# Kernel tuning notes

Hardware: AMD Instinct MI355X
Metric: run time of the kernel (lower is better)

## Reference

```python
import jax, jax.numpy as jnp
import numpy as np

INPUT_DIM = 768
HIDDEN = 64
NUM_CLASSES = 1


def _uniform(key, shape, bound):
    return jax.random.uniform(key, shape, jnp.float32, -bound, bound)


def setup_inputs() -> dict:
    key = jax.random.key(0)
    ks = jax.random.split(key, 16)
    B, T = 128, 512
    bound = 1.0 / np.sqrt(HIDDEN)  # PyTorch RNN init range
    inp = {
        "x": jax.random.normal(ks[0], (B, T, INPUT_DIM), jnp.float32),
        "fixation_num": 1,
        # layer 0: input_dim -> hidden
        "W_ih0": _uniform(ks[1], (HIDDEN, INPUT_DIM), bound),
        "W_hh0": _uniform(ks[2], (HIDDEN, HIDDEN), bound),
        "b_ih0": _uniform(ks[3], (HIDDEN,), bound),
        "b_hh0": _uniform(ks[4], (HIDDEN,), bound),
        # layer 1
        "W_ih1": _uniform(ks[5], (HIDDEN, HIDDEN), bound),
        "W_hh1": _uniform(ks[6], (HIDDEN, HIDDEN), bound),
        "b_ih1": _uniform(ks[7], (HIDDEN,), bound),
        "b_hh1": _uniform(ks[8], (HIDDEN,), bound),
        # layer 2
        "W_ih2": _uniform(ks[9], (HIDDEN, HIDDEN), bound),
        "W_hh2": _uniform(ks[10], (HIDDEN, HIDDEN), bound),
        "b_ih2": _uniform(ks[11], (HIDDEN,), bound),
        "b_hh2": _uniform(ks[12], (HIDDEN,), bound),
        # final linear head
        "fc_w": _uniform(ks[13], (NUM_CLASSES, HIDDEN), bound),
        "fc_b": _uniform(ks[14], (NUM_CLASSES,), bound),
    }
    return inp


def _rnn_layer(x, W_ih, W_hh, b_ih, b_hh):
    # x: [B, T, In] -> hidden sequence [B, T, H]; vanilla tanh RNN, h0 = 0
    pre = jnp.einsum("bti,hi->bth", x, W_ih) + b_ih + b_hh  # input projection for all t
    B = x.shape[0]
    h0 = jnp.zeros((B, W_hh.shape[0]), x.dtype)

    def step(h, p_t):  # p_t: [B, H]
        h = jnp.tanh(p_t + h @ W_hh.T)
        return h, h

    _, hs = jax.lax.scan(step, h0, jnp.swapaxes(pre, 0, 1))  # hs: [T, B, H]
    return jnp.swapaxes(hs, 0, 1)


def reference(x, fixation_num, W_ih0, W_hh0, b_ih0, b_hh0,
              W_ih1, W_hh1, b_ih1, b_hh1,
              W_ih2, W_hh2, b_ih2, b_hh2, fc_w, fc_b):
    # fixation_num is unused by the original forward
    h = _rnn_layer(x, W_ih0, W_hh0, b_ih0, b_hh0)
    h = _rnn_layer(h, W_ih1, W_hh1, b_ih1, b_hh1)
    h = _rnn_layer(h, W_ih2, W_hh2, b_ih2, b_hh2)
    last = h[:, -1, :]  # [B, H]
    return last @ fc_w.T + fc_b  # [B, num_classes]
```

## Files before the change

kernel.cpp:

```cpp
#include <hip/hip_runtime.h>


typedef __fp16 h2_t __attribute__((ext_vector_type(2)));
typedef __fp16 h8_t __attribute__((ext_vector_type(8)));
typedef float  f4_t __attribute__((ext_vector_type(4)));

union F4H  { float4 f; h2_t h[4]; };
union F4H8 { float4 f; h8_t h8; h2_t h2[4]; };
union H8U  { h2_t h2[4]; h8_t h8; };

__device__ __forceinline__ float fdot2(h2_t a, h2_t b, float c) {
    return __builtin_amdgcn_fdot2(a, b, c, false);
}
__device__ __forceinline__ h2_t pack_h2(float x, float y) {
    return __builtin_amdgcn_cvt_pkrtz(x, y);
}
__device__ __forceinline__ float tanh_fast(float x) {
    float e = __expf(2.0f * x);
    return 1.0f - 2.0f * __builtin_amdgcn_rcpf(e + 1.0f);
}

__global__ __launch_bounds__(256) void pack_wih(
    const float* __restrict__ W, h8_t* __restrict__ wp)
{
    const int id = blockIdx.x * 256 + threadIdx.x;
    if (id >= 24 * 4 * 64) return;
    const int l  = id & 63;
    const int nt = (id >> 6) & 3;
    const int c  = id >> 8;
    const float* p = W + (size_t)(nt * 16 + (l & 15)) * 768 + c * 32 + (l >> 4) * 8;
    float4 r0 = *(const float4*)p;
    float4 r1 = *(const float4*)(p + 4);
    H8U u;
    u.h2[0] = pack_h2(r0.x, r0.y); u.h2[1] = pack_h2(r0.z, r0.w);
    u.h2[2] = pack_h2(r1.x, r1.y); u.h2[3] = pack_h2(r1.z, r1.w);
    wp[id] = u.h8;
}

__global__ __launch_bounds__(256) void gemm_pre0(
    const float* __restrict__ x,
    const h8_t* __restrict__ wp,
    const float* __restrict__ bih, const float* __restrict__ bhh,
    float* __restrict__ pre0)
{
    const int tid = threadIdx.x;
    const int wv  = tid >> 6;
    const int l   = tid & 63;
    const int m   = l & 15;
    const int q   = l >> 4;
    const int rowB = blockIdx.x * 64 + wv * 16;

    const float* ax = x + (size_t)(rowB + m) * 768 + q * 8;

    float4 ar[2][2];
    h8_t   bf[2][4];

#pragma unroll
    for (int c = 0; c < 2; ++c) {
        ar[c][0] = *(const float4*)(ax + c * 32);
        ar[c][1] = *(const float4*)(ax + c * 32 + 4);
        const int cb = c * 256 + l;
        bf[c][0] = wp[cb];        bf[c][1] = wp[cb + 64];
        bf[c][2] = wp[cb + 128];  bf[c][3] = wp[cb + 192];
    }

    f4_t acc[4];
#pragma unroll
    for (int nt = 0; nt < 4; ++nt)
#pragma unroll
        for (int i = 0; i < 4; ++i) acc[nt][i] = 0.0f;

#pragma unroll
    for (int it = 0; it < 24; ++it) {
        const int bs = it & 1;
        H8U fa;
        fa.h2[0] = pack_h2(ar[bs][0].x, ar[bs][0].y);
        fa.h2[1] = pack_h2(ar[bs][0].z, ar[bs][0].w);
        fa.h2[2] = pack_h2(ar[bs][1].x, ar[bs][1].y);
        fa.h2[3] = pack_h2(ar[bs][1].z, ar[bs][1].w);
        h8_t fb0 = bf[bs][0], fb1 = bf[bs][1], fb2 = bf[bs][2], fb3 = bf[bs][3];

        if (it + 2 < 24) {
            const int ko = (it + 2) * 32;
            ar[bs][0] = *(const float4*)(ax + ko);
            ar[bs][1] = *(const float4*)(ax + ko + 4);
            const int cb = (it + 2) * 256 + l;
            bf[bs][0] = wp[cb];        bf[bs][1] = wp[cb + 64];
            bf[bs][2] = wp[cb + 128];  bf[bs][3] = wp[cb + 192];
        }

        acc[0] = __builtin_amdgcn_mfma_f32_16x16x32_f16(fa.h8, fb0, acc[0], 0, 0, 0);
        acc[1] = __builtin_amdgcn_mfma_f32_16x16x32_f16(fa.h8, fb1, acc[1], 0, 0, 0);
        acc[2] = __builtin_amdgcn_mfma_f32_16x16x32_f16(fa.h8, fb2, acc[2], 0, 0, 0);
        acc[3] = __builtin_amdgcn_mfma_f32_16x16x32_f16(fa.h8, fb3, acc[3], 0, 0, 0);
    }

    float bn[4];
#pragma unroll
    for (int nt = 0; nt < 4; ++nt) bn[nt] = bih[nt * 16 + m] + bhh[nt * 16 + m];
#pragma unroll
    for (int i = 0; i < 4; ++i) {
        int row = rowB + q * 4 + i;
        float* pr = pre0 + (size_t)row * 64 + m;
#pragma unroll
        for (int nt = 0; nt < 4; ++nt)
            pr[nt * 16] = acc[nt][i] + bn[nt];
    }
}

__device__ __forceinline__ float layer_epoch(
    const __fp16* __restrict__ in0,
    __fp16* __restrict__ self0, int par,
    const h2_t* wB2, const h8_t* wX, float* __restrict__ xb,
    const float* bias4, int j)
{
    __fp16*       selfPar  = self0 + par * 1024;
    const __fp16* selfPrev = self0 + (par ^ 1) * 1024;
    const int mm = j & 15;
    const int q4 = j >> 4;

    F4H8 A0, A1;
    const __fp16* arow = in0 + mm * 64 + q4 * 8;
    A0.f = *(const float4*)arow;
    A1.f = *(const float4*)(arow + 32);

    f4_t xacc[4];
#pragma unroll
    for (int nt = 0; nt < 4; ++nt) {
#pragma unroll
        for (int i = 0; i < 4; ++i) xacc[nt][i] = 0.0f;
        xacc[nt] = __builtin_amdgcn_mfma_f32_16x16x32_f16(
            A0.h8, wX[nt * 2 + 0], xacc[nt], 0, 0, 0);
        xacc[nt] = __builtin_amdgcn_mfma_f32_16x16x32_f16(
            A1.h8, wX[nt * 2 + 1], xacc[nt], 0, 0, 0);
    }
#pragma unroll
    for (int nt = 0; nt < 4; ++nt)
#pragma unroll
        for (int i = 0; i < 4; ++i)
            xb[(q4 * 4 + i) * 64 + nt * 16 + mm] = xacc[nt][i] + bias4[nt];

    float xs[16];
#pragma unroll
    for (int s = 0; s < 16; ++s) xs[s] = xb[s * 64 + j];

    float hN = 0.0f;
#pragma unroll
    for (int s = 0; s < 16; ++s) {
        const __fp16* rc = (s == 0) ? (selfPrev + 15 * 64) : (selfPar + (s - 1) * 64);
        F4H uh[8];
#pragma unroll
        for (int qq = 0; qq < 8; ++qq) uh[qq].f = *(const float4*)(rc + qq * 8);

        float a0 = 0.f, a1 = 0.f, a2 = 0.f, a3 = 0.f;
#pragma unroll
        for (int qq = 0; qq < 8; ++qq) {
            a0 = fdot2(wB2[qq * 4 + 0], uh[qq].h[0], a0);
            a1 = fdot2(wB2[qq * 4 + 1], uh[qq].h[1], a1);
            a2 = fdot2(wB2[qq * 4 + 2], uh[qq].h[2], a2);
            a3 = fdot2(wB2[qq * 4 + 3], uh[qq].h[3], a3);
        }
        hN = tanh_fast((a0 + a1) + (a2 + a3) + xs[s]);
        selfPar[s * 64 + j] = (__fp16)hN;
    }
    return hN;
}

__global__ __launch_bounds__(192, 1) void rnn_fused(
    const float* __restrict__ pre0,
    const float* __restrict__ Whh0,
    const float* __restrict__ Wih1, const float* __restrict__ Whh1,
    const float* __restrict__ bih1, const float* __restrict__ bhh1,
    const float* __restrict__ Wih2, const float* __restrict__ Whh2,
    const float* __restrict__ bih2, const float* __restrict__ bhh2,
    const float* __restrict__ fcw, const float* __restrict__ fcb,
    float* __restrict__ out)
{
    const int tid = threadIdx.x;
    const int g   = tid >> 6;
    const int j   = tid & 63;
    const int b   = blockIdx.x;

    __shared__ __align__(16) __fp16 hb[3][2][16][64];
    __shared__ __align__(16) float  xb2[2][16][64];

    const float* WB = (g == 0) ? Whh0 : ((g == 1) ? Whh1 : Whh2);
    h2_t wB2[32];
#pragma unroll
    for (int i = 0; i < 32; ++i)
        wB2[i] = pack_h2(WB[j * 64 + 2 * i], WB[j * 64 + 2 * i + 1]);

    const float* WX = (g == 1) ? Wih1 : ((g == 2) ? Wih2 : Whh0);
    const int mm = j & 15, q4 = j >> 4;
    h8_t wX[8];
#pragma unroll
    for (int nt = 0; nt < 4; ++nt)
#pragma unroll
        for (int c = 0; c < 2; ++c) {
            const float* p = WX + (nt * 16 + mm) * 64 + c * 32 + q4 * 8;
            float4 r0 = *(const float4*)p;
            float4 r1 = *(const float4*)(p + 4);
            H8U u;
            u.h2[0] = pack_h2(r0.x, r0.y); u.h2[1] = pack_h2(r0.z, r0.w);
            u.h2[2] = pack_h2(r1.x, r1.y); u.h2[3] = pack_h2(r1.z, r1.w);
            wX[nt * 2 + c] = u.h8;
        }

    float bias4[4];
#pragma unroll
    for (int nt = 0; nt < 4; ++nt) {
        const int col = nt * 16 + mm;
        bias4[nt] = (g == 1) ? (bih1[col] + bhh1[col])
                  : ((g == 2) ? (bih2[col] + bhh2[col]) : 0.0f);
    }

#pragma unroll
    for (int i = 0; i < 16; ++i) ((unsigned int*)hb)[tid + 192 * i] = 0u;

    const size_t pbase = (size_t)b * 32768;
    float pc[16], pn[16];
    if (g == 0) {
#pragma unroll
        for (int s = 0; s < 16; ++s) pc[s] = pre0[pbase + s * 64 + j];
    }
    __syncthreads();

    float hLast = 0.0f;

    for (int e = 0; e < 34; ++e) {
        if (g == 0) {
            if (e < 32) {
                if (e < 31) {
#pragma unroll
                    for (int s = 0; s < 16; ++s)
                        pn[s] = pre0[pbase + (size_t)(e + 1) * 1024 + s * 64 + j];
                }
                const int par = e & 1;
#pragma unroll
                for (int s = 0; s < 16; ++s) {
                    const __fp16* rc = (s == 0) ? hb[0][par ^ 1][15] : hb[0][par][s - 1];
                    float a0 = 0.f, a1 = 0.f, a2 = 0.f, a3 = 0.f;
#pragma unroll
                    for (int qq = 0; qq < 8; ++qq) {
                        F4H u; u.f = *(const float4*)&rc[qq * 8];
                        a0 = fdot2(wB2[qq * 4 + 0], u.h[0], a0);
                        a1 = fdot2(wB2[qq * 4 + 1], u.h[1], a1);
                        a2 = fdot2(wB2[qq * 4 + 2], u.h[2], a2);
                        a3 = fdot2(wB2[qq * 4 + 3], u.h[3], a3);
                    }
                    float hN = tanh_fast((a0 + a1) + (a2 + a3) + pc[s]);
                    hb[0][par][s][j] = (__fp16)hN;
                }
#pragma unroll
                for (int s = 0; s < 16; ++s) pc[s] = pn[s];
            }
        } else if (g == 1) {
            if (e >= 1 && e < 33) {
                const int par = (e - 1) & 1;
                layer_epoch(&hb[0][par][0][0], &hb[1][0][0][0], par,
                            wB2, wX, &xb2[0][0][0], bias4, j);
            }
        } else {
            if (e >= 2) {
                const int par = e & 1;
                float hN = layer_epoch(&hb[1][par][0][0], &hb[2][0][0][0], par,
                                       wB2, wX, &xb2[1][0][0], bias4, j);
                if (e == 33) hLast = hN;
            }
        }
        __syncthreads();
    }

    if (g == 2) {
        float v = hLast * fcw[j];
#pragma unroll
        for (int m = 1; m < 64; m <<= 1) v += __shfl_xor(v, m, 64);
        if (j == 0) out[b] = v + fcb[0];
    }
}

extern "C" void kernel_launch(void* const* d_in, const int* in_sizes, int n_in,
                              void* d_out, int out_size, void* d_ws, size_t ws_size,
                              hipStream_t stream) {
    const float* x    = (const float*)d_in[0];
    const float* Wih0 = (const float*)d_in[2];
    const float* Whh0 = (const float*)d_in[3];
    const float* bih0 = (const float*)d_in[4];
    const float* bhh0 = (const float*)d_in[5];
    const float* Wih1 = (const float*)d_in[6];
    const float* Whh1 = (const float*)d_in[7];
    const float* bih1 = (const float*)d_in[8];
    const float* bhh1 = (const float*)d_in[9];
    const float* Wih2 = (const float*)d_in[10];
    const float* Whh2 = (const float*)d_in[11];
    const float* bih2 = (const float*)d_in[12];
    const float* bhh2 = (const float*)d_in[13];
    const float* fcw  = (const float*)d_in[14];
    const float* fcb  = (const float*)d_in[15];
    float* out  = (float*)d_out;
    float* pre0 = (float*)d_ws;
    h8_t* wpack = (h8_t*)((char*)d_ws + (size_t)65536 * 64 * 4);

    pack_wih<<<24, 256, 0, stream>>>(Wih0, wpack);
    gemm_pre0<<<1024, 256, 0, stream>>>(x, wpack, bih0, bhh0, pre0);
    rnn_fused<<<128, 192, 0, stream>>>(pre0, Whh0, Wih1, Whh1, bih1, bhh1,
                                       Wih2, Whh2, bih2, bhh2, fcw, fcb, out);
}
```

Measured before the change: 414.4 us.

## Pack four batch rows per RNN workgroup and deepen x prefetch in GEMM

The recurrent kernel now processes four batch elements per workgroup using 768 threads, with separate shared-memory state per element, launching 32 blocks instead of 128. This is meant to let multiple waves interleave on each CU to hide per-step latency. The input-projection GEMM prefetches x four chunks ahead instead of two to hide global load latency. Risks include register pressure under the larger launch bound, heavier block-wide barriers, and using far fewer CUs.

Result: slower. 507.8 us (+22.5%).

```diff
diff --git a/kernel.cpp b/kernel.cpp
--- a/kernel.cpp
+++ b/kernel.cpp
@@ -52,13 +52,16 @@
 
     const float* ax = x + (size_t)(rowB + m) * 768 + q * 8;
 
-    float4 ar[2][2];
+    float4 ar[4][2];
     h8_t   bf[2][4];
 
 #pragma unroll
-    for (int c = 0; c < 2; ++c) {
+    for (int c = 0; c < 4; ++c) {
         ar[c][0] = *(const float4*)(ax + c * 32);
         ar[c][1] = *(const float4*)(ax + c * 32 + 4);
+    }
+#pragma unroll
+    for (int c = 0; c < 2; ++c) {
         const int cb = c * 256 + l;
         bf[c][0] = wp[cb];        bf[c][1] = wp[cb + 64];
         bf[c][2] = wp[cb + 128];  bf[c][3] = wp[cb + 192];
@@ -72,18 +75,21 @@
 
 #pragma unroll
     for (int it = 0; it < 24; ++it) {
+        const int as = it & 3;
         const int bs = it & 1;
         H8U fa;
-        fa.h2[0] = pack_h2(ar[bs][0].x, ar[bs][0].y);
-        fa.h2[1] = pack_h2(ar[bs][0].z, ar[bs][0].w);
-        fa.h2[2] = pack_h2(ar[bs][1].x, ar[bs][1].y);
-        fa.h2[3] = pack_h2(ar[bs][1].z, ar[bs][1].w);
+        fa.h2[0] = pack_h2(ar[as][0].x, ar[as][0].y);
+        fa.h2[1] = pack_h2(ar[as][0].z, ar[as][0].w);
+        fa.h2[2] = pack_h2(ar[as][1].x, ar[as][1].y);
+        fa.h2[3] = pack_h2(ar[as][1].z, ar[as][1].w);
         h8_t fb0 = bf[bs][0], fb1 = bf[bs][1], fb2 = bf[bs][2], fb3 = bf[bs][3];
 
+        if (it + 4 < 24) {
+            const int ko = (it + 4) * 32;
+            ar[as][0] = *(const float4*)(ax + ko);
+            ar[as][1] = *(const float4*)(ax + ko + 4);
+        }
         if (it + 2 < 24) {
-            const int ko = (it + 2) * 32;
-            ar[bs][0] = *(const float4*)(ax + ko);
-            ar[bs][1] = *(const float4*)(ax + ko + 4);
             const int cb = (it + 2) * 256 + l;
             bf[bs][0] = wp[cb];        bf[bs][1] = wp[cb + 64];
             bf[bs][2] = wp[cb + 128];  bf[bs][3] = wp[cb + 192];
@@ -166,7 +172,7 @@
     return hN;
 }
 
-__global__ __launch_bounds__(192, 1) void rnn_fused(
+__global__ __launch_bounds__(768, 1) void rnn_fused(
     const float* __restrict__ pre0,
     const float* __restrict__ Whh0,
     const float* __restrict__ Wih1, const float* __restrict__ Whh1,
@@ -177,12 +183,14 @@
     float* __restrict__ out)
 {
     const int tid = threadIdx.x;
-    const int g   = tid >> 6;
+    const int w   = tid >> 6;
+    const int g   = w >> 2;
+    const int bi  = w & 3;
     const int j   = tid & 63;
-    const int b   = blockIdx.x;
-
-    __shared__ __align__(16) __fp16 hb[3][2][16][64];
-    __shared__ __align__(16) float  xb2[2][16][64];
+    const int b   = blockIdx.x * 4 + bi;
+
+    __shared__ __align__(16) __fp16 hb[4][3][2][16][64];
+    __shared__ __align__(16) float  xb2[4][2][16][64];
 
     const float* WB = (g == 0) ? Whh0 : ((g == 1) ? Whh1 : Whh2);
     h2_t wB2[32];
@@ -215,7 +223,7 @@
     }
 
 #pragma unroll
-    for (int i = 0; i < 16; ++i) ((unsigned int*)hb)[tid + 192 * i] = 0u;
+    for (int i = 0; i < 16; ++i) ((unsigned int*)hb)[tid + 768 * i] = 0u;
 
     const size_t pbase = (size_t)b * 32768;
     float pc[16], pn[16];
@@ -238,7 +246,8 @@
                 const int par = e & 1;
 #pragma unroll
                 for (int s = 0; s < 16; ++s) {
-                    const __fp16* rc = (s == 0) ? hb[0][par ^ 1][15] : hb[0][par][s - 1];
+                    const __fp16* rc = (s == 0) ? hb[bi][0][par ^ 1][15]
+                                                : hb[bi][0][par][s - 1];
                     float a0 = 0.f, a1 = 0.f, a2 = 0.f, a3 = 0.f;
 #pragma unroll
                     for (int qq = 0; qq < 8; ++qq) {
@@ -249,7 +258,7 @@
                         a3 = fdot2(wB2[qq * 4 + 3], u.h[3], a3);
                     }
                     float hN = tanh_fast((a0 + a1) + (a2 + a3) + pc[s]);
-                    hb[0][par][s][j] = (__fp16)hN;
+                    hb[bi][0][par][s][j] = (__fp16)hN;
                 }
 #pragma unroll
                 for (int s = 0; s < 16; ++s) pc[s] = pn[s];
@@ -257,14 +266,14 @@
         } else if (g == 1) {
             if (e >= 1 && e < 33) {
                 const int par = (e - 1) & 1;
-                layer_epoch(&hb[0][par][0][0], &hb[1][0][0][0], par,
-                            wB2, wX, &xb2[0][0][0], bias4, j);
+                layer_epoch(&hb[bi][0][par][0][0], &hb[bi][1][0][0][0], par,
+                            wB2, wX, &xb2[bi][0][0][0], bias4, j);
             }
         } else {
             if (e >= 2) {
                 const int par = e & 1;
-                float hN = layer_epoch(&hb[1][par][0][0], &hb[2][0][0][0], par,
-                                       wB2, wX, &xb2[1][0][0], bias4, j);
+                float hN = layer_epoch(&hb[bi][1][par][0][0], &hb[bi][2][0][0][0],
+                                       par, wB2, wX, &xb2[bi][1][0][0], bias4, j);
                 if (e == 33) hLast = hN;
             }
         }
@@ -303,6 +312,6 @@
 
     pack_wih<<<24, 256, 0, stream>>>(Wih0, wpack);
     gemm_pre0<<<1024, 256, 0, stream>>>(x, wpack, bih0, bhh0, pre0);
-    rnn_fused<<<128, 192, 0, stream>>>(pre0, Whh0, Wih1, Whh1, bih1, bhh1,
-                                       Wih2, Whh2, bih2, bhh2, fcw, fcb, out);
-}
+    rnn_fused<<<32, 768, 0, stream>>>(pre0, Whh0, Wih1, Whh1, bih1, bhh1,
+                                      Wih2, Whh2, bih2, bhh2, fcw, fcb, out);
+}
```
